# Kernel tuning notes

Measured on AMD Instinct MI355X. Metric: run time of the kernel, lower is better.

The kernel has to match this reference:

```python
import jax, jax.numpy as jnp
import numpy as np

TOPK_FRAC = 0.05
TOPK_MIN = 5
TOPK_MAX = 64


def setup_inputs() -> dict:
    key = jax.random.key(0)
    ks = jax.random.split(key, 8)
    N, H, B = 131072, 256, 512
    x = jax.random.normal(ks[0], (N, H), dtype=jnp.float32)
    batch = jnp.sort(jax.random.randint(ks[1], (N,), 0, B, dtype=jnp.int32))
    W1 = jax.random.normal(ks[2], (H, H // 2), dtype=jnp.float32) * 0.05
    b1 = jax.random.normal(ks[3], (H // 2,), dtype=jnp.float32) * 0.05
    W2 = jax.random.normal(ks[4], (H // 2, 1), dtype=jnp.float32) * 0.05
    b2 = jax.random.normal(ks[5], (1,), dtype=jnp.float32) * 0.05
    Wf = jax.random.normal(ks[6], (4 * H, H), dtype=jnp.float32) * 0.05
    bf = jax.random.normal(ks[7], (H,), dtype=jnp.float32) * 0.05
    return {"x": x, "batch": batch, "W1": W1, "b1": b1, "W2": W2,
            "b2": b2, "Wf": Wf, "bf": bf, "num_graphs": B}


def _forward(x, batch, W1, b1, W2, b2, Wf, bf, B):
    N = x.shape[0]
    # attention scores per node: MLP -> scalar
    s = (jax.nn.relu(x @ W1 + b1) @ W2 + b2)[:, 0]  # [N]
    # pyg_softmax: segment-wise stable softmax over nodes of each graph
    seg_max = jax.ops.segment_max(s, batch, num_segments=B)
    seg_max = jnp.where(jnp.isfinite(seg_max), seg_max, 0.0)  # guard empty segs
    e = jnp.exp(s - seg_max[batch])
    denom = jax.ops.segment_sum(e, batch, num_segments=B)
    w = e / denom[batch]                                    # [N]
    # pools
    x_attn = jax.ops.segment_sum(x * w[:, None], batch, num_segments=B)
    counts = jax.ops.segment_sum(jnp.ones((N,), jnp.int32), batch, num_segments=B)
    cnt_f = jnp.maximum(counts, 1).astype(x.dtype)
    x_mean = jax.ops.segment_sum(x, batch, num_segments=B) / cnt_f[:, None]
    x_max = jax.ops.segment_max(x, batch, num_segments=B)
    x_max = jnp.where(counts[:, None] > 0, x_max, 0.0)
    # per-graph dynamic k
    n = counts
    k = jnp.maximum(TOPK_MIN, jnp.ceil(TOPK_FRAC * n.astype(jnp.float32)).astype(jnp.int32))
    k = jnp.minimum(jnp.minimum(k, TOPK_MAX), n)            # [B]
    # fused segment top-k mean: sort nodes by (batch asc, w desc), keep rank<k
    order = jnp.lexsort((-w, batch))
    starts = jnp.concatenate([jnp.zeros((1,), jnp.int32), jnp.cumsum(counts)[:-1].astype(jnp.int32)])
    bs = batch[order]
    rank = jnp.arange(N, dtype=jnp.int32) - starts[bs]
    sel = (rank < k[bs]).astype(x.dtype)
    x_topk = jax.ops.segment_sum(x[order] * sel[:, None], bs, num_segments=B)
    x_topk = x_topk / jnp.maximum(k, 1).astype(x.dtype)[:, None]
    g = jax.nn.relu(jnp.concatenate([x_mean, x_attn, x_max, x_topk], axis=1) @ Wf + bf)
    return g


def reference(x, batch, W1, b1, W2, b2, Wf, bf, num_graphs):
    return _forward(x, batch, W1, b1, W2, b2, Wf, bf, num_graphs)
```

## Files before the change

kernel.cpp:

```cpp
#include <hip/hip_runtime.h>
#include <math.h>

#define N_NODES 131072
#define H 256
#define HH 128
#define B_GRAPHS 512

typedef __attribute__((ext_vector_type(8))) short bfrag8;
typedef __attribute__((ext_vector_type(16))) float f32x16;

__device__ __forceinline__ float bfhi(float v) {
  return __builtin_bit_cast(float, __builtin_bit_cast(unsigned, v) & 0xFFFF0000u);
}

__global__ void k_prep_w1(const float* __restrict__ W1, ushort* __restrict__ W1f) {
  const int idx = blockIdx.x * 256 + threadIdx.x;
  const int k = idx >> 7, c = idx & 127;
  const float v = W1[idx];
  const float r = v - bfhi(v);
  const float r2 = r - bfhi(r);
  const int ks = k >> 4, g = (k >> 3) & 1, e = k & 7;
  const int base = (((ks)*2 + g) * 128 + c) * 8 + e;
  const int plane = 16 * 2 * 128 * 8;
  W1f[0 * plane + base] = (ushort)(__builtin_bit_cast(unsigned, v) >> 16);
  W1f[1 * plane + base] = (ushort)(__builtin_bit_cast(unsigned, r) >> 16);
  W1f[2 * plane + base] = (ushort)(__builtin_bit_cast(unsigned, r2) >> 16);
}

__global__ void k_seg_bounds(const int* __restrict__ batch, int* __restrict__ seg_start,
                             int N, int B) {
  int b = blockIdx.x * blockDim.x + threadIdx.x;
  if (b > B) return;
  int lo = 0, hi = N;
  while (lo < hi) {
    int mid = (lo + hi) >> 1;
    if (batch[mid] < b) lo = mid + 1; else hi = mid;
  }
  seg_start[b] = lo;
}

#define PROD(sa, sb)                                                                        \
  do {                                                                                      \
    acc[0][0] = __builtin_amdgcn_mfma_f32_32x32x16_bf16(af[sa][0], bb[sub][sb][0],          \
                                                        acc[0][0], 0, 0, 0);                \
    acc[0][1] = __builtin_amdgcn_mfma_f32_32x32x16_bf16(af[sa][0], bb[sub][sb][1],          \
                                                        acc[0][1], 0, 0, 0);                \
    acc[1][0] = __builtin_amdgcn_mfma_f32_32x32x16_bf16(af[sa][1], bb[sub][sb][0],          \
                                                        acc[1][0], 0, 0, 0);                \
    acc[1][1] = __builtin_amdgcn_mfma_f32_32x32x16_bf16(af[sa][1], bb[sub][sb][1],          \
                                                        acc[1][1], 0, 0, 0);                \
  } while (0)

__device__ __forceinline__ void split8(const float4 v0, const float4 v1,
                                       bfrag8& p1, bfrag8& p2, bfrag8& p3) {
  const float vals[8] = {v0.x, v0.y, v0.z, v0.w, v1.x, v1.y, v1.z, v1.w};
#pragma unroll
  for (int e = 0; e < 8; ++e) {
    const float v = vals[e];
    const float r = v - bfhi(v);
    const float r2 = r - bfhi(r);
    p1[e] = (short)(__builtin_bit_cast(unsigned, v) >> 16);
    p2[e] = (short)(__builtin_bit_cast(unsigned, r) >> 16);
    p3[e] = (short)(__builtin_bit_cast(unsigned, r2) >> 16);
  }
}

__global__ __launch_bounds__(256, 3) void k_score_mfma(
    const float* __restrict__ x, const ushort* __restrict__ W1f,
    const float* __restrict__ b1, const float* __restrict__ W2,
    const float* __restrict__ b2, float* __restrict__ s_out) {
  __shared__ float smem[8192];
  const int t = threadIdx.x;
  const int lane = t & 63;
  const int w = t >> 6;
  const int wr = w >> 1, wc = w & 1;
  const int nl = lane & 31, g = lane >> 5;
  const int node0 = blockIdx.x * 128;

  const int srow = t >> 3, schunk = t & 7;
  const int swz = (schunk ^ (srow & 7)) << 2;

  const f32x16 zero = (f32x16)0.0f;
  f32x16 acc[2][2];
  acc[0][0] = zero; acc[0][1] = zero; acc[1][0] = zero; acc[1][1] = zero;

#pragma unroll
  for (int q = 0; q < 4; ++q) {
    const float4 v = *(const float4*)(x + (size_t)(node0 + q * 32 + srow) * H + schunk * 4);
    *(float4*)&smem[(q * 32 + srow) * 32 + swz] = v;
  }
  __syncthreads();

#pragma unroll
  for (int it = 0; it < 8; ++it) {
    const int kc = it * 32;
    const int cur = it & 1;
    float4 gx[4];
    if (it < 7) {
#pragma unroll
      for (int q = 0; q < 4; ++q)
        gx[q] = *(const float4*)(x + (size_t)(node0 + q * 32 + srow) * H + kc + 32 + schunk * 4);
    }
    bfrag8 bb[2][3][2];
#pragma unroll
    for (int sub = 0; sub < 2; ++sub)
#pragma unroll
      for (int s = 0; s < 3; ++s)
#pragma unroll
        for (int j = 0; j < 2; ++j) {
          const int ks = it * 2 + sub;
          bb[sub][s][j] = *(const bfrag8*)(W1f + (size_t)(((s * 16 + ks) * 2 + g) * 128 +
                                                          (wc * 64 + j * 32 + nl)) * 8);
        }
#pragma unroll
    for (int sub = 0; sub < 2; ++sub) {
      const int k0 = sub * 16;
      bfrag8 af[3][2];
#pragma unroll
      for (int i = 0; i < 2; ++i) {
        const int R = wr * 64 + i * 32 + nl;
        const int c0 = (k0 >> 2) + g * 2;
        const float4 v0 = *(const float4*)&smem[cur * 4096 + R * 32 + ((c0 ^ (R & 7)) << 2)];
        const float4 v1 =
            *(const float4*)&smem[cur * 4096 + R * 32 + (((c0 + 1) ^ (R & 7)) << 2)];
        split8(v0, v1, af[0][i], af[1][i], af[2][i]);
      }
      PROD(0, 0); PROD(1, 0); PROD(0, 1); PROD(1, 1); PROD(2, 0); PROD(0, 2);
    }
    if (it < 7) {
#pragma unroll
      for (int q = 0; q < 4; ++q)
        *(float4*)&smem[(cur ^ 1) * 4096 + (q * 32 + srow) * 32 + swz] = gx[q];
    }
    __syncthreads();
  }

  float* part = smem;
  const int col0 = wc * 64 + nl;
  const float b1v0 = b1[col0], b1v1 = b1[col0 + 32];
  const float w2v0 = W2[col0], w2v1 = W2[col0 + 32];
#pragma unroll
  for (int i = 0; i < 2; ++i) {
#pragma unroll
    for (int r = 0; r < 16; ++r) {
      const int nodeL = wr * 64 + i * 32 + (r & 3) + 8 * (r >> 2) + 4 * g;
      const float h0 = acc[i][0][r] + b1v0;
      const float h1 = acc[i][1][r] + b1v1;
      const float p = fmaxf(h0, 0.f) * w2v0 + fmaxf(h1, 0.f) * w2v1;
      part[nodeL * 64 + wc * 32 + nl] = p;
    }
  }
  __syncthreads();
  if (t < 128) {
    float sv = b2[0];
#pragma unroll 8
    for (int cc = 0; cc < 64; ++cc) {
      const int c2 = (cc + t) & 63;
      sv += part[t * 64 + c2];
    }
    s_out[node0 + t] = sv;
  }
}

__global__ __launch_bounds__(512) void k_pool_fused(const float* __restrict__ x,
                                                    const float* __restrict__ s,
                                                    const int* __restrict__ seg_start,
                                                    float* __restrict__ pooled) {
  const int b = blockIdx.x;
  const int t = threadIdx.x;
  const int start = seg_start[b];
  const int end = seg_start[b + 1];
  const int n = end - start;

  __shared__ float s_lds[1024];
  __shared__ float red[512];
  __shared__ float thr_sh;
  __shared__ int thri_sh;
  __shared__ float r4[8][264];

  const bool fits = (n <= 1024);
  if (fits) {
    for (int i = t; i < n; i += 512) s_lds[i] = s[start + i];
  }
  __syncthreads();
  const float* sseg = fits ? s_lds : (s + start);

  float m = -INFINITY;
  for (int i = t; i < n; i += 512) m = fmaxf(m, sseg[i]);
  red[t] = m;
  __syncthreads();
  for (int off = 256; off > 0; off >>= 1) {
    if (t < off) red[t] = fmaxf(red[t], red[t + off]);
    __syncthreads();
  }
  const float smax = red[0];
  __syncthreads();
  float d = 0.f;
  for (int i = t; i < n; i += 512) d += __expf(sseg[i] - smax);
  red[t] = d;
  __syncthreads();
  for (int off = 256; off > 0; off >>= 1) {
    if (t < off) red[t] += red[t + off];
    __syncthreads();
  }
  const float denom = red[0];
  __syncthreads();
  const float inv_denom = (denom > 0.f) ? 1.f / denom : 0.f;

  int k = 0;
  if (n > 0) {
    k = (int)ceilf(0.05f * (float)n);
    if (k < 5) k = 5;
    if (k > 64) k = 64;
    if (k > n) k = n;
  }

  if (t < 64) {
    float pk = INFINITY;
    int pidx = -1;
    for (int r = 0; r < k; ++r) {
      float bk = -INFINITY;
      int bi = 0x7fffffff;
      for (int i = t; i < n; i += 64) {
        const float si = sseg[i];
        const int gi = start + i;
        const bool below = (si < pk) || (si == pk && gi > pidx);
        if (below && (si > bk || (si == bk && gi < bi))) { bk = si; bi = gi; }
      }
#pragma unroll
      for (int off = 32; off > 0; off >>= 1) {
        const float ok = __shfl_xor(bk, off);
        const int oi = __shfl_xor(bi, off);
        if (ok > bk || (ok == bk && oi < bi)) { bk = ok; bi = oi; }
      }
      pk = bk;
      pidx = bi;
    }
    if (t == 0) {
      thr_sh = (k > 0) ? pk : INFINITY;
      thri_sh = (k > 0) ? pidx : -1;
    }
  }
  __syncthreads();
  const float thr = thr_sh;
  const int thri = thri_sh;

  const int fq = t & 63;
  const int sub = t >> 6;
  float mean[4] = {0.f, 0.f, 0.f, 0.f};
  float attn[4] = {0.f, 0.f, 0.f, 0.f};
  float tk[4] = {0.f, 0.f, 0.f, 0.f};
  float mx[4] = {-INFINITY, -INFINITY, -INFINITY, -INFINITY};
  for (int i = sub; i < n; i += 8) {
    const float si = sseg[i];
    const float wi = __expf(si - smax);
    const int gi = start + i;
    const bool sel = (si > thr) || (si == thr && gi <= thri);
    const float4 xv = *reinterpret_cast<const float4*>(x + (size_t)gi * H + fq * 4);
    mean[0] += xv.x; mean[1] += xv.y; mean[2] += xv.z; mean[3] += xv.w;
    attn[0] = fmaf(xv.x, wi, attn[0]);
    attn[1] = fmaf(xv.y, wi, attn[1]);
    attn[2] = fmaf(xv.z, wi, attn[2]);
    attn[3] = fmaf(xv.w, wi, attn[3]);
    mx[0] = fmaxf(mx[0], xv.x);
    mx[1] = fmaxf(mx[1], xv.y);
    mx[2] = fmaxf(mx[2], xv.z);
    mx[3] = fmaxf(mx[3], xv.w);
    if (sel) {
      tk[0] += xv.x; tk[1] += xv.y; tk[2] += xv.z; tk[3] += xv.w;
    }
  }
  float* po = pooled + (size_t)b * 1024;
  const float invn = 1.f / (float)(n > 0 ? n : 1);
  const float invk = (k > 0) ? 1.f / (float)k : 0.f;
  *reinterpret_cast<float4*>(&r4[sub][fq * 4]) = make_float4(mean[0], mean[1], mean[2], mean[3]);
  __syncthreads();
  if (t < 256) {
    float tot = 0.f;
#pragma unroll
    for (int q = 0; q < 8; ++q) tot += r4[q][t];
    po[t] = tot * invn;
  }
  __syncthreads();
  *reinterpret_cast<float4*>(&r4[sub][fq * 4]) = make_float4(attn[0], attn[1], attn[2], attn[3]);
  __syncthreads();
  if (t < 256) {
    float tot = 0.f;
#pragma unroll
    for (int q = 0; q < 8; ++q) tot += r4[q][t];
    po[256 + t] = tot * inv_denom;
  }
  __syncthreads();
  *reinterpret_cast<float4*>(&r4[sub][fq * 4]) = make_float4(mx[0], mx[1], mx[2], mx[3]);
  __syncthreads();
  if (t < 256) {
    float tot = -INFINITY;
#pragma unroll
    for (int q = 0; q < 8; ++q) tot = fmaxf(tot, r4[q][t]);
    po[512 + t] = (n > 0) ? tot : 0.f;
  }
  __syncthreads();
  *reinterpret_cast<float4*>(&r4[sub][fq * 4]) = make_float4(tk[0], tk[1], tk[2], tk[3]);
  __syncthreads();
  if (t < 256) {
    float tot = 0.f;
#pragma unroll
    for (int q = 0; q < 8; ++q) tot += r4[q][t];
    po[768 + t] = tot * invk;
  }
}

__global__ __launch_bounds__(256) void k_gemm(const float* __restrict__ pooled,
                                              const float* __restrict__ Wf,
                                              float* __restrict__ gacc) {
  const int t = threadIdx.x;
  const int r0 = blockIdx.x * 8;
  const int kc0 = blockIdx.y * 128;
  __shared__ float ps[8][132];
  {
    const int r = t >> 5;
    const int c = (t & 31) << 2;
    *reinterpret_cast<float4*>(&ps[r][c]) =
        *reinterpret_cast<const float4*>(pooled + (size_t)(r0 + r) * 1024 + kc0 + c);
  }
  __syncthreads();
  float acc[8];
#pragma unroll
  for (int r = 0; r < 8; ++r) acc[r] = 0.f;
#pragma unroll 4
  for (int c = 0; c < 128; ++c) {
    const float wf = Wf[(size_t)(kc0 + c) * 256 + t];
#pragma unroll
    for (int r = 0; r < 8; ++r) acc[r] = fmaf(ps[r][c], wf, acc[r]);
  }
  float* go = gacc + ((size_t)blockIdx.y * B_GRAPHS + r0) * 256;
#pragma unroll
  for (int r = 0; r < 8; ++r) go[r * 256 + t] = acc[r];
}

__global__ __launch_bounds__(256) void k_out(const float* __restrict__ gacc,
                                             const float* __restrict__ bf,
                                             float* __restrict__ out) {
  const int i = blockIdx.x * 256 + threadIdx.x;
  float v = bf[i & 255];
#pragma unroll
  for (int ks = 0; ks < 8; ++ks) v += gacc[(size_t)ks * (B_GRAPHS * 256) + i];
  out[i] = fmaxf(v, 0.f);
}

extern "C" void kernel_launch(void* const* d_in, const int* in_sizes, int n_in,
                              void* d_out, int out_size, void* d_ws, size_t ws_size,
                              hipStream_t stream) {
  const float* x  = (const float*)d_in[0];
  const int* batch = (const int*)d_in[1];
  const float* W1 = (const float*)d_in[2];
  const float* b1 = (const float*)d_in[3];
  const float* W2 = (const float*)d_in[4];
  const float* b2 = (const float*)d_in[5];
  const float* Wf = (const float*)d_in[6];
  const float* bf = (const float*)d_in[7];
  const int N = in_sizes[1];
  const int B = B_GRAPHS;

  float* ws = (float*)d_ws;
  float* s = ws;
  int* seg_start = (int*)(ws + N);
  float* pooled = ws + N + 1024;
  float* gacc = pooled + (size_t)B * 1024;
  ushort* W1f = (ushort*)(gacc + (size_t)8 * B * 256);

  k_prep_w1<<<dim3(128), dim3(256), 0, stream>>>(W1, W1f);
  k_seg_bounds<<<dim3((B + 1 + 255) / 256), dim3(256), 0, stream>>>(batch, seg_start, N, B);
  k_score_mfma<<<dim3(N / 128), dim3(256), 0, stream>>>(x, W1f, b1, W2, b2, s);
  k_pool_fused<<<dim3(B), dim3(512), 0, stream>>>(x, s, seg_start, pooled);
  k_gemm<<<dim3(B / 8, 8), dim3(256), 0, stream>>>(pooled, Wf, gacc);
  k_out<<<dim3((B * 256) / 256), dim3(256), 0, stream>>>(gacc, bf, (float*)d_out);
}
```

Before: 119.5 us.

## Replace bf16x3 split GEMM with scaled fp16x2 split in score kernel

The score MLP's first matmul changes from a three-way bf16 split (6 MFMAs per tile step) to a two-way fp16 split: a main half plus a residual scaled by 4096. This needs 3 MFMAs per step, with the residual products kept in a separate accumulator. Inputs are converted once when staged into shared memory, and W1 is staged transposed through LDS, where before it was read directly from global memory. This cuts MFMA count and per-fragment conversion work. In exchange it uses more LDS, lowers the occupancy hint from 3 to 2, and relies on fp16 range and precision holding for the inputs.

After: 124.7 us. 4.4% more time.

```diff
diff --git a/kernel.cpp b/kernel.cpp
--- a/kernel.cpp
+++ b/kernel.cpp
@@ -6,25 +6,25 @@
 #define HH 128
 #define B_GRAPHS 512
 
-typedef __attribute__((ext_vector_type(8))) short bfrag8;
+typedef __attribute__((ext_vector_type(8))) _Float16 half8;
+typedef __attribute__((ext_vector_type(2))) _Float16 half2v;
 typedef __attribute__((ext_vector_type(16))) float f32x16;
 
-__device__ __forceinline__ float bfhi(float v) {
-  return __builtin_bit_cast(float, __builtin_bit_cast(unsigned, v) & 0xFFFF0000u);
-}
-
-__global__ void k_prep_w1(const float* __restrict__ W1, ushort* __restrict__ W1f) {
+__device__ __forceinline__ uint packh(_Float16 h0, _Float16 h1) {
+  half2v t;
+  t[0] = h0; t[1] = h1;
+  return __builtin_bit_cast(uint, t);
+}
+
+__global__ void k_prep_w1(const float* __restrict__ W1, ushort* __restrict__ W1h) {
   const int idx = blockIdx.x * 256 + threadIdx.x;
   const int k = idx >> 7, c = idx & 127;
   const float v = W1[idx];
-  const float r = v - bfhi(v);
-  const float r2 = r - bfhi(r);
-  const int ks = k >> 4, g = (k >> 3) & 1, e = k & 7;
-  const int base = (((ks)*2 + g) * 128 + c) * 8 + e;
-  const int plane = 16 * 2 * 128 * 8;
-  W1f[0 * plane + base] = (ushort)(__builtin_bit_cast(unsigned, v) >> 16);
-  W1f[1 * plane + base] = (ushort)(__builtin_bit_cast(unsigned, r) >> 16);
-  W1f[2 * plane + base] = (ushort)(__builtin_bit_cast(unsigned, r2) >> 16);
+  const _Float16 h1 = (_Float16)v;
+  const float r = (v - (float)h1) * 4096.f;
+  const _Float16 h2 = (_Float16)r;
+  W1h[0 * 32768 + c * 256 + k] = __builtin_bit_cast(ushort, h1);
+  W1h[1 * 32768 + c * 256 + k] = __builtin_bit_cast(ushort, h2);
 }
 
 __global__ void k_seg_bounds(const int* __restrict__ batch, int* __restrict__ seg_start,
@@ -39,37 +39,11 @@
   seg_start[b] = lo;
 }
 
-#define PROD(sa, sb)                                                                        \
-  do {                                                                                      \
-    acc[0][0] = __builtin_amdgcn_mfma_f32_32x32x16_bf16(af[sa][0], bb[sub][sb][0],          \
-                                                        acc[0][0], 0, 0, 0);                \
-    acc[0][1] = __builtin_amdgcn_mfma_f32_32x32x16_bf16(af[sa][0], bb[sub][sb][1],          \
-                                                        acc[0][1], 0, 0, 0);                \
-    acc[1][0] = __builtin_amdgcn_mfma_f32_32x32x16_bf16(af[sa][1], bb[sub][sb][0],          \
-                                                        acc[1][0], 0, 0, 0);                \
-    acc[1][1] = __builtin_amdgcn_mfma_f32_32x32x16_bf16(af[sa][1], bb[sub][sb][1],          \
-                                                        acc[1][1], 0, 0, 0);                \
-  } while (0)
-
-__device__ __forceinline__ void split8(const float4 v0, const float4 v1,
-                                       bfrag8& p1, bfrag8& p2, bfrag8& p3) {
-  const float vals[8] = {v0.x, v0.y, v0.z, v0.w, v1.x, v1.y, v1.z, v1.w};
-#pragma unroll
-  for (int e = 0; e < 8; ++e) {
-    const float v = vals[e];
-    const float r = v - bfhi(v);
-    const float r2 = r - bfhi(r);
-    p1[e] = (short)(__builtin_bit_cast(unsigned, v) >> 16);
-    p2[e] = (short)(__builtin_bit_cast(unsigned, r) >> 16);
-    p3[e] = (short)(__builtin_bit_cast(unsigned, r2) >> 16);
-  }
-}
-
-__global__ __launch_bounds__(256, 3) void k_score_mfma(
-    const float* __restrict__ x, const ushort* __restrict__ W1f,
+__global__ __launch_bounds__(256, 2) void k_score_mfma(
+    const float* __restrict__ x, const ushort* __restrict__ W1h,
     const float* __restrict__ b1, const float* __restrict__ W2,
     const float* __restrict__ b2, float* __restrict__ s_out) {
-  __shared__ float smem[8192];
+  __shared__ ushort smem[20480];
   const int t = threadIdx.x;
   const int lane = t & 63;
   const int w = t >> 6;
@@ -77,65 +51,99 @@
   const int nl = lane & 31, g = lane >> 5;
   const int node0 = blockIdx.x * 128;
 
-  const int srow = t >> 3, schunk = t & 7;
-  const int swz = (schunk ^ (srow & 7)) << 2;
+  const int srow = t >> 1;
+  const int shalf = t & 1;
 
   const f32x16 zero = (f32x16)0.0f;
-  f32x16 acc[2][2];
-  acc[0][0] = zero; acc[0][1] = zero; acc[1][0] = zero; acc[1][1] = zero;
-
-#pragma unroll
-  for (int q = 0; q < 4; ++q) {
-    const float4 v = *(const float4*)(x + (size_t)(node0 + q * 32 + srow) * H + schunk * 4);
-    *(float4*)&smem[(q * 32 + srow) * 32 + swz] = v;
-  }
-  __syncthreads();
+  f32x16 acc1[2][2], acc2[2][2];
+#pragma unroll
+  for (int i = 0; i < 2; ++i)
+#pragma unroll
+    for (int j = 0; j < 2; ++j) { acc1[i][j] = zero; acc2[i][j] = zero; }
+
+  float4 gxA[4];
+  uint4 gB[2][2];
+
+  const float* xrow = x + (size_t)(node0 + srow) * H + shalf * 16;
+  const ushort* wrow = W1h + srow * 256 + shalf * 16;
+
+#pragma unroll
+  for (int q = 0; q < 4; ++q) gxA[q] = *(const float4*)(xrow + q * 4);
+#pragma unroll
+  for (int p = 0; p < 2; ++p) {
+    gB[p][0] = *(const uint4*)(wrow + p * 32768);
+    gB[p][1] = *(const uint4*)(wrow + p * 32768 + 8);
+  }
 
 #pragma unroll
   for (int it = 0; it < 8; ++it) {
-    const int kc = it * 32;
-    const int cur = it & 1;
-    float4 gx[4];
+    {
+      uint mainw[8], residw[8];
+#pragma unroll
+      for (int q = 0; q < 4; ++q) {
+        const float vv[4] = {gxA[q].x, gxA[q].y, gxA[q].z, gxA[q].w};
+#pragma unroll
+        for (int p = 0; p < 2; ++p) {
+          const float v0 = vv[2 * p], v1 = vv[2 * p + 1];
+          const _Float16 h0 = (_Float16)v0, h1 = (_Float16)v1;
+          const float r0 = (v0 - (float)h0) * 4096.f;
+          const float r1 = (v1 - (float)h1) * 4096.f;
+          mainw[2 * q + p] = packh(h0, h1);
+          residw[2 * q + p] = packh((_Float16)r0, (_Float16)r1);
+        }
+      }
+      uint4* a0 = (uint4*)&smem[0 * 5120 + srow * 40 + shalf * 16];
+      uint4* a1 = (uint4*)&smem[1 * 5120 + srow * 40 + shalf * 16];
+      a0[0] = make_uint4(mainw[0], mainw[1], mainw[2], mainw[3]);
+      a0[1] = make_uint4(mainw[4], mainw[5], mainw[6], mainw[7]);
+      a1[0] = make_uint4(residw[0], residw[1], residw[2], residw[3]);
+      a1[1] = make_uint4(residw[4], residw[5], residw[6], residw[7]);
+#pragma unroll
+      for (int p = 0; p < 2; ++p) {
+        uint4* bp = (uint4*)&smem[10240 + p * 5120 + srow * 40 + shalf * 16];
+        bp[0] = gB[p][0];
+        bp[1] = gB[p][1];
+      }
+    }
+    __syncthreads();
     if (it < 7) {
-#pragma unroll
-      for (int q = 0; q < 4; ++q)
-        gx[q] = *(const float4*)(x + (size_t)(node0 + q * 32 + srow) * H + kc + 32 + schunk * 4);
-    }
-    bfrag8 bb[2][3][2];
-#pragma unroll
-    for (int sub = 0; sub < 2; ++sub)
-#pragma unroll
-      for (int s = 0; s < 3; ++s)
+      const int kc = (it + 1) * 32;
+#pragma unroll
+      for (int q = 0; q < 4; ++q) gxA[q] = *(const float4*)(xrow + kc + q * 4);
+#pragma unroll
+      for (int p = 0; p < 2; ++p) {
+        gB[p][0] = *(const uint4*)(wrow + p * 32768 + kc);
+        gB[p][1] = *(const uint4*)(wrow + p * 32768 + kc + 8);
+      }
+    }
+#pragma unroll
+    for (int sub = 0; sub < 2; ++sub) {
+      half8 a[2][2], b[2][2];
+#pragma unroll
+      for (int p = 0; p < 2; ++p) {
+#pragma unroll
+        for (int i = 0; i < 2; ++i)
+          a[p][i] = *(const half8*)&smem[p * 5120 + (wr * 64 + i * 32 + nl) * 40 +
+                                         sub * 16 + g * 8];
+#pragma unroll
+        for (int j = 0; j < 2; ++j)
+          b[p][j] = *(const half8*)&smem[10240 + p * 5120 + (wc * 64 + j * 32 + nl) * 40 +
+                                         sub * 16 + g * 8];
+      }
+#pragma unroll
+      for (int i = 0; i < 2; ++i)
 #pragma unroll
         for (int j = 0; j < 2; ++j) {
-          const int ks = it * 2 + sub;
-          bb[sub][s][j] = *(const bfrag8*)(W1f + (size_t)(((s * 16 + ks) * 2 + g) * 128 +
-                                                          (wc * 64 + j * 32 + nl)) * 8);
+          acc1[i][j] = __builtin_amdgcn_mfma_f32_32x32x16_f16(a[0][i], b[0][j], acc1[i][j], 0, 0, 0);
+          acc2[i][j] = __builtin_amdgcn_mfma_f32_32x32x16_f16(a[0][i], b[1][j], acc2[i][j], 0, 0, 0);
+          acc2[i][j] = __builtin_amdgcn_mfma_f32_32x32x16_f16(a[1][i], b[0][j], acc2[i][j], 0, 0, 0);
         }
-#pragma unroll
-    for (int sub = 0; sub < 2; ++sub) {
-      const int k0 = sub * 16;
-      bfrag8 af[3][2];
-#pragma unroll
-      for (int i = 0; i < 2; ++i) {
-        const int R = wr * 64 + i * 32 + nl;
-        const int c0 = (k0 >> 2) + g * 2;
-        const float4 v0 = *(const float4*)&smem[cur * 4096 + R * 32 + ((c0 ^ (R & 7)) << 2)];
-        const float4 v1 =
-            *(const float4*)&smem[cur * 4096 + R * 32 + (((c0 + 1) ^ (R & 7)) << 2)];
-        split8(v0, v1, af[0][i], af[1][i], af[2][i]);
-      }
-      PROD(0, 0); PROD(1, 0); PROD(0, 1); PROD(1, 1); PROD(2, 0); PROD(0, 2);
-    }
-    if (it < 7) {
-#pragma unroll
-      for (int q = 0; q < 4; ++q)
-        *(float4*)&smem[(cur ^ 1) * 4096 + (q * 32 + srow) * 32 + swz] = gx[q];
     }
     __syncthreads();
   }
 
-  float* part = smem;
+  float* part = (float*)smem;
+  const float inv4096 = 2.44140625e-4f;
   const int col0 = wc * 64 + nl;
   const float b1v0 = b1[col0], b1v1 = b1[col0 + 32];
   const float w2v0 = W2[col0], w2v1 = W2[col0 + 32];
@@ -144,8 +152,8 @@
 #pragma unroll
     for (int r = 0; r < 16; ++r) {
       const int nodeL = wr * 64 + i * 32 + (r & 3) + 8 * (r >> 2) + 4 * g;
-      const float h0 = acc[i][0][r] + b1v0;
-      const float h1 = acc[i][1][r] + b1v1;
+      const float h0 = acc1[i][0][r] + acc2[i][0][r] * inv4096 + b1v0;
+      const float h1 = acc1[i][1][r] + acc2[i][1][r] * inv4096 + b1v1;
       const float p = fmaxf(h0, 0.f) * w2v0 + fmaxf(h1, 0.f) * w2v1;
       part[nodeL * 64 + wc * 32 + nl] = p;
     }
@@ -367,11 +375,11 @@
   int* seg_start = (int*)(ws + N);
   float* pooled = ws + N + 1024;
   float* gacc = pooled + (size_t)B * 1024;
-  ushort* W1f = (ushort*)(gacc + (size_t)8 * B * 256);
-
-  k_prep_w1<<<dim3(128), dim3(256), 0, stream>>>(W1, W1f);
+  ushort* W1h = (ushort*)(gacc + (size_t)8 * B * 256);
+
+  k_prep_w1<<<dim3(128), dim3(256), 0, stream>>>(W1, W1h);
   k_seg_bounds<<<dim3((B + 1 + 255) / 256), dim3(256), 0, stream>>>(batch, seg_start, N, B);
-  k_score_mfma<<<dim3(N / 128), dim3(256), 0, stream>>>(x, W1f, b1, W2, b2, s);
+  k_score_mfma<<<dim3(N / 128), dim3(256), 0, stream>>>(x, W1h, b1, W2, b2, s);
   k_pool_fused<<<dim3(B), dim3(512), 0, stream>>>(x, s, seg_start, pooled);
   k_gemm<<<dim3(B / 8, 8), dim3(256), 0, stream>>>(pooled, Wf, gacc);
   k_out<<<dim3((B * 256) / 256), dim3(256), 0, stream>>>(gacc, bf, (float*)d_out);
```
